# Kernel optimization log

Measured on AMD Instinct MI355X. Metric: run time of the kernel, lower is better.

The kernel has to match this reference:

```python
import jax, jax.numpy as jnp
import numpy as np

INPUT_DIM = 1024
NUM_HEADS = 16
HEAD_DIM = INPUT_DIM // NUM_HEADS


def setup_inputs() -> dict:
    key = jax.random.key(0)
    ks = jax.random.split(key, 9)
    d = INPUT_DIM
    s = 1.0 / np.sqrt(d)
    x = jax.random.normal(ks[0], (2, 2048, d), dtype=jnp.float32)
    # nn.Linear default init ~ U(-1/sqrt(in), 1/sqrt(in)); weights stored as (out, in), we keep (in, out)
    Wq = jax.random.uniform(ks[1], (d, d), jnp.float32, -s, s)
    bq = jax.random.uniform(ks[2], (d,), jnp.float32, -s, s)
    Wk = jax.random.uniform(ks[3], (d, d), jnp.float32, -s, s)
    bk = jax.random.uniform(ks[4], (d,), jnp.float32, -s, s)
    Wv = jax.random.uniform(ks[5], (d, d), jnp.float32, -s, s)
    bv = jax.random.uniform(ks[6], (d,), jnp.float32, -s, s)
    Wo = jax.random.uniform(ks[7], (d, d), jnp.float32, -s, s)
    bo = jax.random.uniform(ks[8], (d,), jnp.float32, -s, s)
    return {"x": x, "Wq": Wq, "bq": bq, "Wk": Wk, "bk": bk, "Wv": Wv, "bv": bv, "Wo": Wo, "bo": bo}


def reference(x, Wq, bq, Wk, bk, Wv, bv, Wo, bo):
    b, t, d = x.shape
    h, hd = NUM_HEADS, HEAD_DIM
    # projections -> [b, h, t, hd]
    q = (x @ Wq + bq).reshape(b, t, h, hd).transpose(0, 2, 1, 3)
    k = (x @ Wk + bk).reshape(b, t, h, hd).transpose(0, 2, 1, 3)
    v = (x @ Wv + bv).reshape(b, t, h, hd).transpose(0, 2, 1, 3)
    scores = jnp.einsum('bhqd,bhkd->bhqk', q, k) / jnp.sqrt(jnp.float32(hd))
    probs = jax.nn.softmax(scores, axis=-1)
    out = jnp.einsum('bhqk,bhkd->bhqd', probs, v)
    out = out.transpose(0, 2, 1, 3).reshape(b, t, d)
    return out @ Wo + bo
```

## Files before the change

### kernel.cpp

```cpp
#include <hip/hip_runtime.h>
#include <math.h>


#define BATCH 2
#define SEQ   2048
#define DIM   1024
#define NHEAD 16
#define HDIM  64
#define MROWS (BATCH * SEQ)
#define BH    (BATCH * NHEAD)
#define NSPLIT 2
#define TILES_PER_SPLIT (SEQ / 64 / NSPLIT)

typedef __attribute__((ext_vector_type(4))) float     floatx4;
typedef __attribute__((ext_vector_type(4))) float     float4v;
typedef __attribute__((ext_vector_type(8))) _Float16  half8;
typedef __attribute__((ext_vector_type(4))) _Float16  half4;
typedef __attribute__((ext_vector_type(2))) __fp16    fp16x2;

#define SOFT_C 5.77078016f
#define QSCALE 0.18033688f

#if __has_builtin(__builtin_amdgcn_exp2f)
#define EXP2F(x) __builtin_amdgcn_exp2f(x)
#else
#define EXP2F(x) exp2f(x)
#endif

__device__ __forceinline__ void gload16(const void* g, void* l) {
    __builtin_amdgcn_global_load_lds(
        (const __attribute__((address_space(1))) unsigned int*)g,
        (__attribute__((address_space(3))) unsigned int*)l, 16, 0, 0);
}

__device__ __forceinline__ unsigned pk2(float a, float b) {
    fp16x2 v = __builtin_amdgcn_cvt_pkrtz(a, b);
    return __builtin_bit_cast(unsigned, v);
}

__global__ __launch_bounds__(256) void prep(
    const float* __restrict__ x,
    const float* __restrict__ Wq, const float* __restrict__ Wk,
    const float* __restrict__ Wv, const float* __restrict__ Wo,
    _Float16* __restrict__ xh,
    _Float16* __restrict__ Wqt, _Float16* __restrict__ Wkt,
    _Float16* __restrict__ Wvt, _Float16* __restrict__ Wot)
{
    const int tid = threadIdx.x;
    if (blockIdx.z == 4) {
        const int bid = blockIdx.y * 16 + blockIdx.x;
        #pragma unroll
        for (int it = 0; it < 8; ++it) {
            const size_t i = (((size_t)it * 256 + bid) * 256 + tid) * 8;
            float4v a = *(const float4v*)(x + i);
            float4v b = *(const float4v*)(x + i + 4);
            half8 o;
            #pragma unroll
            for (int c = 0; c < 4; ++c) { o[c] = (_Float16)a[c]; o[4+c] = (_Float16)b[c]; }
            *(half8*)(xh + i) = o;
        }
        return;
    }
    __shared__ float tile[64][65];
    const float* W; _Float16* o;
    switch (blockIdx.z) {
        case 0: W = Wq; o = Wqt; break;
        case 1: W = Wk; o = Wkt; break;
        case 2: W = Wv; o = Wvt; break;
        default: W = Wo; o = Wot; break;
    }
    const int n0 = blockIdx.x * 64, k0 = blockIdx.y * 64;
    #pragma unroll
    for (int p = 0; p < 16; ++p) {
        int idx = tid + p * 256;
        int r = idx >> 6, c = idx & 63;
        tile[r][c] = W[(size_t)(k0 + r) * DIM + n0 + c];
    }
    __syncthreads();
    #pragma unroll
    for (int p = 0; p < 16; ++p) {
        int idx = tid + p * 256;
        int r = idx >> 6, c = idx & 63;
        o[(size_t)(n0 + r) * DIM + k0 + c] = (_Float16)tile[c][r];
    }
}

__device__ __forceinline__ void gemm_core16(
    const _Float16* __restrict__ Ap, const _Float16* __restrict__ Bp,
    int m0, int n0, _Float16* AL, _Float16* BL, floatx4 acc[4][4])
{
    const int tid  = threadIdx.x;
    const int wave = tid >> 6;
    const int lane = tid & 63;
    const int li   = lane & 15;
    const int quad = lane >> 4;
    const int wm   = (wave >> 1) * 64;
    const int wn   = (wave & 1) * 64;

    for (int kt = 0; kt < DIM / 64; ++kt) {
        __syncthreads();
        const int k0 = kt * 64;
        #pragma unroll
        for (int p = 0; p < 4; ++p) {
            int s = tid + p * 256;
            int r = s >> 3, ks = s & 7;
            int kg = (ks ^ (r & 7)) << 3;
            int ldsb = (wave * 64 + p * 256) * 8;
            gload16(Ap + (size_t)(m0 + r) * DIM + k0 + kg, AL + ldsb);
            gload16(Bp + (size_t)(n0 + r) * DIM + k0 + kg, BL + ldsb);
        }
        __syncthreads();

        half8 a[4][2], b[4][2];
        #pragma unroll
        for (int i = 0; i < 4; ++i) {
            int ra = (wm + i * 16 + li) << 6;
            int rb = (wn + i * 16 + li) << 6;
            #pragma unroll
            for (int h = 0; h < 2; ++h) {
                a[i][h] = *(const half8*)(AL + ra + (((h * 4 + quad) ^ (li & 7)) << 3));
                b[i][h] = *(const half8*)(BL + rb + (((h * 4 + quad) ^ (li & 7)) << 3));
            }
        }
        #pragma unroll
        for (int i = 0; i < 4; ++i)
            #pragma unroll
            for (int j = 0; j < 4; ++j) {
                acc[i][j] = __builtin_amdgcn_mfma_f32_16x16x32_f16(a[i][0], b[j][0], acc[i][j], 0, 0, 0);
                acc[i][j] = __builtin_amdgcn_mfma_f32_16x16x32_f16(a[i][1], b[j][1], acc[i][j], 0, 0, 0);
            }
    }
}

__global__ __launch_bounds__(256, 2) void qkv_mfma(
    const _Float16* __restrict__ xh,
    const _Float16* __restrict__ Wqt, const _Float16* __restrict__ Wkt,
    const _Float16* __restrict__ Wvt,
    const float* __restrict__ bq, const float* __restrict__ bk,
    const float* __restrict__ bv,
    _Float16* __restrict__ Qh, _Float16* __restrict__ Kh,
    _Float16* __restrict__ Vth)
{
    __shared__ __align__(16) _Float16 SH[128 * 136];
    _Float16* AL = SH;
    _Float16* BL = SH + 128 * 64;

    const int z = blockIdx.z;
    const _Float16* Bp; const float* bias;
    if (z == 0)      { Bp = Wqt; bias = bq; }
    else if (z == 1) { Bp = Wkt; bias = bk; }
    else             { Bp = Wvt; bias = bv; }

    const int m0 = blockIdx.y * 128, n0 = blockIdx.x * 128;

    floatx4 acc[4][4];
    #pragma unroll
    for (int i = 0; i < 4; ++i)
        #pragma unroll
        for (int j = 0; j < 4; ++j) acc[i][j] = (floatx4){0.f, 0.f, 0.f, 0.f};

    gemm_core16(xh, Bp, m0, n0, AL, BL, acc);

    const int tid = threadIdx.x, wave = tid >> 6, lane = tid & 63;
    const int li = lane & 15, quad = lane >> 4;
    const int wm = (wave >> 1) * 64, wn = (wave & 1) * 64;
    const int bb = m0 >> 11, t0 = m0 & 2047;

    if (z != 2) {
        _Float16* out = (z == 0) ? Qh : Kh;
        const float sc = (z == 0) ? QSCALE : 1.0f;
        #pragma unroll
        for (int i = 0; i < 4; ++i)
            #pragma unroll
            for (int j = 0; j < 4; ++j) {
                int n = n0 + wn + j * 16 + li;
                int h = n >> 6, hd = n & 63;
                float b_ = bias[n];
                #pragma unroll
                for (int r = 0; r < 4; ++r) {
                    int m = m0 + wm + i * 16 + quad * 4 + r;
                    int t = m & 2047;
                    out[(((size_t)(bb * NHEAD + h) * SEQ) + t) * HDIM + hd] =
                        (_Float16)((acc[i][j][r] + b_) * sc);
                }
            }
    } else {
        __syncthreads();
        #pragma unroll
        for (int i = 0; i < 4; ++i)
            #pragma unroll
            for (int j = 0; j < 4; ++j) {
                int n = wn + j * 16 + li;
                float b_ = bias[n0 + n];
                half4 w;
                #pragma unroll
                for (int r = 0; r < 4; ++r) w[r] = (_Float16)(acc[i][j][r] + b_);
                *(half4*)(SH + n * 136 + wm + i * 16 + quad * 4) = w;
            }
        __syncthreads();
        #pragma unroll
        for (int p = 0; p < 8; ++p) {
            int idx = p * 256 + tid;
            int v = idx >> 4, c8 = (idx & 15) * 8;
            half8 w = *(const half8*)(SH + v * 136 + c8);
            int n = n0 + v;
            int h = n >> 6, hd = n & 63;
            *(half8*)(Vth + ((size_t)(bb * NHEAD + h) * HDIM + hd) * SEQ + t0 + c8) = w;
        }
    }
}

#define LDP 72

__global__ __launch_bounds__(256) void attn(
    const _Float16* __restrict__ Q, const _Float16* __restrict__ K,
    const _Float16* __restrict__ Vt,
    _Float16* __restrict__ Op0, _Float16* __restrict__ Op1,
    float* __restrict__ rsb)
{
    __shared__ __align__(16) _Float16 Ks[64 * 64];
    __shared__ __align__(16) _Float16 Vs[64 * 64];
    __shared__ __align__(16) _Float16 Pt[4][32 * LDP];

    const int tid  = threadIdx.x;
    const int wave = tid >> 6;
    const int lane = tid & 63;
    const int li   = lane & 15;
    const int quad = lane >> 4;
    const int bh   = blockIdx.y;
    const int q0   = blockIdx.x * 128;
    const int z    = blockIdx.z;
    const int b    = bh >> 4, h = bh & 15;

    half8 qa[2][2];
    #pragma unroll
    for (int nq = 0; nq < 2; ++nq) {
        size_t qrow = ((size_t)bh * SEQ + q0 + wave * 32 + nq * 16 + li) * HDIM;
        qa[nq][0] = *(const half8*)(Q + qrow + quad * 8);
        qa[nq][1] = *(const half8*)(Q + qrow + 32 + quad * 8);
    }

    half8 onesA;
    {
        _Float16 v = (li == 0) ? (_Float16)1.0f : (_Float16)0.0f;
        #pragma unroll
        for (int c = 0; c < 8; ++c) onesA[c] = v;
    }

    floatx4 O[4][2];
    floatx4 rsacc[2];
    #pragma unroll
    for (int nq = 0; nq < 2; ++nq) {
        rsacc[nq] = (floatx4){0.f, 0.f, 0.f, 0.f};
        #pragma unroll
        for (int i = 0; i < 4; ++i) O[i][nq] = (floatx4){0.f, 0.f, 0.f, 0.f};
    }

    const _Float16* Kbh = K  + (size_t)bh * SEQ * HDIM;
    const _Float16* Vbh = Vt + (size_t)bh * HDIM * SEQ;
    _Float16* Pw = Pt[wave];

    for (int kt = z * TILES_PER_SPLIT; kt < (z + 1) * TILES_PER_SPLIT; ++kt) {
        __syncthreads();
        {
            const _Float16* Kg = Kbh + (size_t)kt * 64 * HDIM;
            const _Float16* Vg = Vbh + kt * 64;
            #pragma unroll
            for (int p = 0; p < 2; ++p) {
                int s = tid + p * 256;
                int r = s >> 3, ks = s & 7;
                int kg = (ks ^ (r & 7)) << 3;
                int ldsb = (wave * 64 + p * 256) * 8;
                gload16(Kg + r * HDIM + kg, (_Float16*)Ks + ldsb);
                gload16(Vg + (size_t)r * SEQ + kg, (_Float16*)Vs + ldsb);
            }
        }
        __syncthreads();

        #pragma unroll
        for (int mb = 0; mb < 4; ++mb) {
            int row = (mb * 16 + li) << 6;
            half8 a0 = *(const half8*)(Ks + row + ((quad ^ (li & 7)) << 3));
            half8 a1 = *(const half8*)(Ks + row + (((quad + 4) ^ (li & 7)) << 3));
            #pragma unroll
            for (int nq = 0; nq < 2; ++nq) {
                floatx4 st = (floatx4){0.f, 0.f, 0.f, 0.f};
                st = __builtin_amdgcn_mfma_f32_16x16x32_f16(a0, qa[nq][0], st, 0, 0, 0);
                st = __builtin_amdgcn_mfma_f32_16x16x32_f16(a1, qa[nq][1], st, 0, 0, 0);
                float p0 = EXP2F(st[0] - SOFT_C);
                float p1 = EXP2F(st[1] - SOFT_C);
                float p2 = EXP2F(st[2] - SOFT_C);
                float p3 = EXP2F(st[3] - SOFT_C);
                uint2 w; w.x = pk2(p0, p1); w.y = pk2(p2, p3);
                *(uint2*)(Pw + (nq * 16 + li) * LDP + mb * 16 + quad * 4) = w;
            }
        }

        half8 pb[2][2];
        #pragma unroll
        for (int nq = 0; nq < 2; ++nq) {
            pb[nq][0] = *(const half8*)(Pw + (nq * 16 + li) * LDP + quad * 8);
            pb[nq][1] = *(const half8*)(Pw + (nq * 16 + li) * LDP + 32 + quad * 8);
        }
        #pragma unroll
        for (int nq = 0; nq < 2; ++nq) {
            rsacc[nq] = __builtin_amdgcn_mfma_f32_16x16x32_f16(onesA, pb[nq][0], rsacc[nq], 0, 0, 0);
            rsacc[nq] = __builtin_amdgcn_mfma_f32_16x16x32_f16(onesA, pb[nq][1], rsacc[nq], 0, 0, 0);
        }
        #pragma unroll
        for (int mb = 0; mb < 4; ++mb) {
            int row = (mb * 16 + li) << 6;
            half8 v0 = *(const half8*)(Vs + row + ((quad ^ (li & 7)) << 3));
            half8 v1 = *(const half8*)(Vs + row + (((quad + 4) ^ (li & 7)) << 3));
            #pragma unroll
            for (int nq = 0; nq < 2; ++nq) {
                O[mb][nq] = __builtin_amdgcn_mfma_f32_16x16x32_f16(v0, pb[nq][0], O[mb][nq], 0, 0, 0);
                O[mb][nq] = __builtin_amdgcn_mfma_f32_16x16x32_f16(v1, pb[nq][1], O[mb][nq], 0, 0, 0);
            }
        }
    }

    if (quad == 0) {
        #pragma unroll
        for (int nq = 0; nq < 2; ++nq)
            rsb[((size_t)z * BH + bh) * SEQ + q0 + wave * 32 + nq * 16 + li] = rsacc[nq][0];
    }

    _Float16* Op = (z == 0) ? Op0 : Op1;

    #pragma unroll
    for (int mb = 0; mb < 4; ++mb)
        #pragma unroll
        for (int nq = 0; nq < 2; ++nq) {
            uint2 w;
            w.x = pk2(O[mb][nq][0], O[mb][nq][1]);
            w.y = pk2(O[mb][nq][2], O[mb][nq][3]);
            *(uint2*)(Pw + (nq * 16 + li) * LDP + mb * 16 + quad * 4) = w;
        }
    #pragma unroll
    for (int p = 0; p < 4; ++p) {
        int idx = p * 64 + lane;
        int qq = idx >> 3, c8 = (idx & 7) * 8;
        half8 v = *(const half8*)(Pw + qq * LDP + c8);
        size_t row = (size_t)b * SEQ + q0 + wave * 32 + qq;
        *(half8*)(Op + row * DIM + h * HDIM + c8) = v;
    }
}

__global__ __launch_bounds__(256) void combine(
    const _Float16* __restrict__ Op0, const _Float16* __restrict__ Op1,
    const float* __restrict__ rsb, _Float16* __restrict__ Ctx)
{
    const size_t idx8 = (size_t)blockIdx.x * 256 + threadIdx.x;
    const int m = (int)(idx8 >> 7);
    const int c = (int)(idx8 & 127);
    const int h = c >> 3;
    const int b = m >> 11, t = m & 2047;
    const size_t rsi = (size_t)(b * NHEAD + h) * SEQ + t;
    const float r0 = rsb[rsi];
    const float r1 = rsb[(size_t)BH * SEQ + rsi];
    const float inv = 1.0f / (r0 + r1);
    const size_t off = idx8 * 8;
    half8 o0 = *(const half8*)(Op0 + off);
    half8 o1 = *(const half8*)(Op1 + off);
    half8 o;
    #pragma unroll
    for (int r = 0; r < 8; ++r)
        o[r] = (_Float16)(((float)o0[r] + (float)o1[r]) * inv);
    *(half8*)(Ctx + off) = o;
}

__global__ __launch_bounds__(256, 2) void out_mfma(
    const _Float16* __restrict__ Ctx, const _Float16* __restrict__ Wot,
    const float* __restrict__ bo, float* __restrict__ out)
{
    __shared__ __align__(16) _Float16 AL[128 * 64];
    __shared__ __align__(16) _Float16 BL[128 * 64];

    const int m0 = blockIdx.y * 128, n0 = blockIdx.x * 128;

    floatx4 acc[4][4];
    #pragma unroll
    for (int i = 0; i < 4; ++i)
        #pragma unroll
        for (int j = 0; j < 4; ++j) acc[i][j] = (floatx4){0.f, 0.f, 0.f, 0.f};

    gemm_core16(Ctx, Wot, m0, n0, AL, BL, acc);

    const int tid = threadIdx.x, wave = tid >> 6, lane = tid & 63;
    const int li = lane & 15, quad = lane >> 4;
    const int wm = (wave >> 1) * 64, wn = (wave & 1) * 64;

    #pragma unroll
    for (int i = 0; i < 4; ++i)
        #pragma unroll
        for (int j = 0; j < 4; ++j) {
            int n = n0 + wn + j * 16 + li;
            float b_ = bo[n];
            #pragma unroll
            for (int r = 0; r < 4; ++r) {
                int m = m0 + wm + i * 16 + quad * 4 + r;
                out[(size_t)m * DIM + n] = acc[i][j][r] + b_;
            }
        }
}

extern "C" void kernel_launch(void* const* d_in, const int* in_sizes, int n_in,
                              void* d_out, int out_size, void* d_ws, size_t ws_size,
                              hipStream_t stream) {
    const float* x  = (const float*)d_in[0];
    const float* Wq = (const float*)d_in[1];
    const float* bq = (const float*)d_in[2];
    const float* Wk = (const float*)d_in[3];
    const float* bk = (const float*)d_in[4];
    const float* Wv = (const float*)d_in[5];
    const float* bv = (const float*)d_in[6];
    const float* Wo = (const float*)d_in[7];
    const float* bo = (const float*)d_in[8];
    float* out = (float*)d_out;

    const size_t PX = (size_t)MROWS * DIM;
    const size_t PW = (size_t)DIM * DIM;
    _Float16* xh  = (_Float16*)d_ws;
    _Float16* Wqt = xh + PX;
    _Float16* Wkt = Wqt + PW;
    _Float16* Wvt = Wkt + PW;
    _Float16* Wot = Wvt + PW;
    _Float16* Qh  = Wot + PW;
    _Float16* Kh  = Qh + PX;
    _Float16* Op1 = Kh + PX;
    _Float16* Vth = Op1 + PX;

    _Float16* Op0 = xh;
    float*    rsb = (float*)Wqt;
    _Float16* Ctx = xh;

    prep<<<dim3(16, 16, 5), 256, 0, stream>>>(
        x, Wq, Wk, Wv, Wo, xh, Wqt, Wkt, Wvt, Wot);

    qkv_mfma<<<dim3(DIM / 128, MROWS / 128, 3), 256, 0, stream>>>(
        xh, Wqt, Wkt, Wvt, bq, bk, bv, Qh, Kh, Vth);

    attn<<<dim3(SEQ / 128, BH, NSPLIT), 256, 0, stream>>>(
        Qh, Kh, Vth, Op0, Op1, rsb);

    combine<<<dim3(PX / 8 / 256), 256, 0, stream>>>(Op0, Op1, rsb, Ctx);

    out_mfma<<<dim3(DIM / 128, MROWS / 128), 256, 0, stream>>>(
        Ctx, Wot, bo, out);
}
```

Baseline: 198.8 us.

## Drop split-K attention and combine kernel, normalize in attention epilogue

Attention now processes the full key range in one block instead of two splits, so the partial outputs, row-sum buffer and separate combine kernel go away. Normalization by the row sum is done in the epilogue through a lane shuffle. The softmax offset is folded into the MFMA accumulator's initial value, and qkv/out GEMM launch bounds rise to 3 waves per SIMD. The attention grid halves to 512 blocks, which reduces parallelism and lengthens each block's serial loop over keys.

```diff
diff --git a/kernel.cpp b/kernel.cpp
--- a/kernel.cpp
+++ b/kernel.cpp
@@ -9,8 +9,6 @@
 #define HDIM  64
 #define MROWS (BATCH * SEQ)
 #define BH    (BATCH * NHEAD)
-#define NSPLIT 2
-#define TILES_PER_SPLIT (SEQ / 64 / NSPLIT)
 
 typedef __attribute__((ext_vector_type(4))) float     floatx4;
 typedef __attribute__((ext_vector_type(4))) float     float4v;
@@ -132,7 +130,7 @@
     }
 }
 
-__global__ __launch_bounds__(256, 2) void qkv_mfma(
+__global__ __launch_bounds__(256, 3) void qkv_mfma(
     const _Float16* __restrict__ xh,
     const _Float16* __restrict__ Wqt, const _Float16* __restrict__ Wkt,
     const _Float16* __restrict__ Wvt,
@@ -214,9 +212,7 @@
 
 __global__ __launch_bounds__(256) void attn(
     const _Float16* __restrict__ Q, const _Float16* __restrict__ K,
-    const _Float16* __restrict__ Vt,
-    _Float16* __restrict__ Op0, _Float16* __restrict__ Op1,
-    float* __restrict__ rsb)
+    const _Float16* __restrict__ Vt, _Float16* __restrict__ Ctx)
 {
     __shared__ __align__(16) _Float16 Ks[64 * 64];
     __shared__ __align__(16) _Float16 Vs[64 * 64];
@@ -229,7 +225,6 @@
     const int quad = lane >> 4;
     const int bh   = blockIdx.y;
     const int q0   = blockIdx.x * 128;
-    const int z    = blockIdx.z;
     const int b    = bh >> 4, h = bh & 15;
 
     half8 qa[2][2];
@@ -260,7 +255,7 @@
     const _Float16* Vbh = Vt + (size_t)bh * HDIM * SEQ;
     _Float16* Pw = Pt[wave];
 
-    for (int kt = z * TILES_PER_SPLIT; kt < (z + 1) * TILES_PER_SPLIT; ++kt) {
+    for (int kt = 0; kt < SEQ / 64; ++kt) {
         __syncthreads();
         {
             const _Float16* Kg = Kbh + (size_t)kt * 64 * HDIM;
@@ -284,14 +279,12 @@
             half8 a1 = *(const half8*)(Ks + row + (((quad + 4) ^ (li & 7)) << 3));
             #pragma unroll
             for (int nq = 0; nq < 2; ++nq) {
-                floatx4 st = (floatx4){0.f, 0.f, 0.f, 0.f};
+                floatx4 st = (floatx4){-SOFT_C, -SOFT_C, -SOFT_C, -SOFT_C};
                 st = __builtin_amdgcn_mfma_f32_16x16x32_f16(a0, qa[nq][0], st, 0, 0, 0);
                 st = __builtin_amdgcn_mfma_f32_16x16x32_f16(a1, qa[nq][1], st, 0, 0, 0);
-                float p0 = EXP2F(st[0] - SOFT_C);
-                float p1 = EXP2F(st[1] - SOFT_C);
-                float p2 = EXP2F(st[2] - SOFT_C);
-                float p3 = EXP2F(st[3] - SOFT_C);
-                uint2 w; w.x = pk2(p0, p1); w.y = pk2(p2, p3);
+                uint2 w;
+                w.x = pk2(EXP2F(st[0]), EXP2F(st[1]));
+                w.y = pk2(EXP2F(st[2]), EXP2F(st[3]));
                 *(uint2*)(Pw + (nq * 16 + li) * LDP + mb * 16 + quad * 4) = w;
             }
         }
@@ -320,21 +313,20 @@
         }
     }
 
-    if (quad == 0) {
-        #pragma unroll
-        for (int nq = 0; nq < 2; ++nq)
-            rsb[((size_t)z * BH + bh) * SEQ + q0 + wave * 32 + nq * 16 + li] = rsacc[nq][0];
-    }
-
-    _Float16* Op = (z == 0) ? Op0 : Op1;
+    float inv[2];
+    #pragma unroll
+    for (int nq = 0; nq < 2; ++nq) {
+        float r = __shfl(rsacc[nq][0], li, 64);
+        inv[nq] = 1.0f / r;
+    }
 
     #pragma unroll
     for (int mb = 0; mb < 4; ++mb)
         #pragma unroll
         for (int nq = 0; nq < 2; ++nq) {
             uint2 w;
-            w.x = pk2(O[mb][nq][0], O[mb][nq][1]);
-            w.y = pk2(O[mb][nq][2], O[mb][nq][3]);
+            w.x = pk2(O[mb][nq][0] * inv[nq], O[mb][nq][1] * inv[nq]);
+            w.y = pk2(O[mb][nq][2] * inv[nq], O[mb][nq][3] * inv[nq]);
             *(uint2*)(Pw + (nq * 16 + li) * LDP + mb * 16 + quad * 4) = w;
         }
     #pragma unroll
@@ -343,34 +335,11 @@
         int qq = idx >> 3, c8 = (idx & 7) * 8;
         half8 v = *(const half8*)(Pw + qq * LDP + c8);
         size_t row = (size_t)b * SEQ + q0 + wave * 32 + qq;
-        *(half8*)(Op + row * DIM + h * HDIM + c8) = v;
-    }
-}
-
-__global__ __launch_bounds__(256) void combine(
-    const _Float16* __restrict__ Op0, const _Float16* __restrict__ Op1,
-    const float* __restrict__ rsb, _Float16* __restrict__ Ctx)
-{
-    const size_t idx8 = (size_t)blockIdx.x * 256 + threadIdx.x;
-    const int m = (int)(idx8 >> 7);
-    const int c = (int)(idx8 & 127);
-    const int h = c >> 3;
-    const int b = m >> 11, t = m & 2047;
-    const size_t rsi = (size_t)(b * NHEAD + h) * SEQ + t;
-    const float r0 = rsb[rsi];
-    const float r1 = rsb[(size_t)BH * SEQ + rsi];
-    const float inv = 1.0f / (r0 + r1);
-    const size_t off = idx8 * 8;
-    half8 o0 = *(const half8*)(Op0 + off);
-    half8 o1 = *(const half8*)(Op1 + off);
-    half8 o;
-    #pragma unroll
-    for (int r = 0; r < 8; ++r)
-        o[r] = (_Float16)(((float)o0[r] + (float)o1[r]) * inv);
-    *(half8*)(Ctx + off) = o;
-}
-
-__global__ __launch_bounds__(256, 2) void out_mfma(
+        *(half8*)(Ctx + row * DIM + h * HDIM + c8) = v;
+    }
+}
+
+__global__ __launch_bounds__(256, 3) void out_mfma(
     const _Float16* __restrict__ Ctx, const _Float16* __restrict__ Wot,
     const float* __restrict__ bo, float* __restrict__ out)
 {
@@ -428,11 +397,8 @@
     _Float16* Wot = Wvt + PW;
     _Float16* Qh  = Wot + PW;
     _Float16* Kh  = Qh + PX;
-    _Float16* Op1 = Kh + PX;
-    _Float16* Vth = Op1 + PX;
-
-    _Float16* Op0 = xh;
-    float*    rsb = (float*)Wqt;
+    _Float16* Vth = Kh + PX;
+
     _Float16* Ctx = xh;
 
     prep<<<dim3(16, 16, 5), 256, 0, stream>>>(
@@ -441,10 +407,7 @@
     qkv_mfma<<<dim3(DIM / 128, MROWS / 128, 3), 256, 0, stream>>>(
         xh, Wqt, Wkt, Wvt, bq, bk, bv, Qh, Kh, Vth);
 
-    attn<<<dim3(SEQ / 128, BH, NSPLIT), 256, 0, stream>>>(
-        Qh, Kh, Vth, Op0, Op1, rsb);
-
-    combine<<<dim3(PX / 8 / 256), 256, 0, stream>>>(Op0, Op1, rsb, Ctx);
+    attn<<<dim3(SEQ / 128, BH), 256, 0, stream>>>(Qh, Kh, Vth, Ctx);
 
     out_mfma<<<dim3(DIM / 128, MROWS / 128), 256, 0, stream>>>(
         Ctx, Wot, bo, out);
```

New measurement: 201.2 us. Within noise of the previous version (+1.2%).
